# Kernel tuning notes

Measured on AMD Instinct MI355X. Metric: run time of the kernel, lower is better.

The kernel has to match this reference:

```python
import jax, jax.numpy as jnp
import numpy as np

B, DIM, RES, NS, ITERS = 64, 256, 32, 8, 5
NTOK = RES * RES
HID = max(DIM, 128)
EPS = 1e-08
SCALE = DIM ** -0.5


def build_grid(res):
    r = [np.linspace(0.0, 1.0, num=n) for n in (res, res)]
    g = np.stack(np.meshgrid(*r, sparse=False, indexing='ij'), axis=-1)
    g = g.reshape(1, res, res, 2).astype(np.float32)
    return jnp.asarray(np.concatenate([g, 1.0 - g], axis=-1))  # [1,res,res,4]


def ln(x, g, b, eps=1e-5):
    m = x.mean(-1, keepdims=True)
    v = ((x - m) ** 2).mean(-1, keepdims=True)
    return (x - m) / jnp.sqrt(v + eps) * g + b


def ln2(x, g, b, eps=1e-5):  # LayerNorm over last two dims ([ntokens, dim])
    m = x.mean((-2, -1), keepdims=True)
    v = ((x - m) ** 2).mean((-2, -1), keepdims=True)
    return (x - m) / jnp.sqrt(v + eps) * g + b


def lin(x, W, b):
    return x @ W.T + b


def gru_cell(x, h, W_ih, W_hh, b_ih, b_hh):
    gi = x @ W_ih.T + b_ih
    gh = h @ W_hh.T + b_hh
    ir, iz, i_n = jnp.split(gi, 3, axis=-1)
    hr, hz, h_n = jnp.split(gh, 3, axis=-1)
    r = jax.nn.sigmoid(ir + hr)
    z = jax.nn.sigmoid(iz + hz)
    n = jnp.tanh(i_n + r * h_n)
    return (1.0 - z) * n + z * h


def setup_inputs() -> dict:
    key = jax.random.key(0)
    ks = jax.random.split(key, 32)
    p = lambda i, shape, s=0.02: (jax.random.normal(ks[i], shape, dtype=jnp.float32) * s)
    d = {
        'inputs': jax.random.normal(ks[0], (B, DIM, RES, RES), dtype=jnp.float32),
        'init_noise': jax.random.normal(ks[1], (B, NS, DIM), dtype=jnp.float32),
        'W_pos': p(2, (DIM, 4)), 'b_pos': jnp.zeros((DIM,)),
        'g_enc': jnp.ones((NTOK, DIM)), 'b_enc': jnp.zeros((NTOK, DIM)),
        'W_m1': p(3, (DIM, DIM)), 'b_m1': jnp.zeros((DIM,)),
        'W_m2': p(4, (DIM, DIM)), 'b_m2': jnp.zeros((DIM,)),
        'g_in': jnp.ones((DIM,)), 'b_in': jnp.zeros((DIM,)),
        'Wq': p(5, (DIM, DIM)), 'bq': jnp.zeros((DIM,)),
        'Wk': p(6, (DIM, DIM)), 'bk': jnp.zeros((DIM,)),
        'Wv': p(7, (DIM, DIM)), 'bv': jnp.zeros((DIM,)),
        'W_ih': p(8, (3 * DIM, DIM)), 'W_hh': p(9, (3 * DIM, DIM)),
        'b_ih': jnp.zeros((3 * DIM,)), 'b_hh': jnp.zeros((3 * DIM,)),
        'g_s': jnp.ones((DIM,)), 'b_s': jnp.zeros((DIM,)),
        'g_ff': jnp.ones((DIM,)), 'b_ff': jnp.zeros((DIM,)),
        'W_f1': p(10, (HID, DIM)), 'b_f1': jnp.zeros((HID,)),
        'W_f2': p(11, (DIM, HID)), 'b_f2': jnp.zeros((DIM,)),
        'mu': p(12, (1, 1, DIM), 0.1), 'sigma': p(13, (1, 1, DIM), 0.1),
    }
    return d


def _forward(inputs, init_noise, W_pos, b_pos, g_enc, b_enc, W_m1, b_m1, W_m2, b_m2,
             g_in, b_in, Wq, bq, Wk, bk, Wv, bv, W_ih, W_hh, b_ih, b_hh,
             g_s, b_s, g_ff, b_ff, W_f1, b_f1, W_f2, b_f2, mu, sigma):
    grid = build_grid(RES)  # [1,RES,RES,4]
    # encoder transformation (position=True)
    f = jnp.transpose(inputs, (0, 2, 3, 1))               # [B,RES,RES,DIM]
    f = f + lin(grid, W_pos, b_pos)                       # soft position embed
    f = f.reshape(B, NTOK, DIM)
    f = ln2(f, g_enc, b_enc)                              # LayerNorm([ntokens, dim])
    f = jnp.maximum(lin(f, W_m1, b_m1), 0.0)
    f = jnp.maximum(lin(f, W_m2, b_m2), 0.0)
    f = ln(f, g_in, b_in)                                 # norm_input
    k = lin(f, Wk, bk)
    v = lin(f, Wv, bv)

    def step(slots):
        s = ln(slots, g_s, b_s)
        q = lin(s, Wq, bq)
        dots = jnp.einsum('bid,bjd->bij', q, k) * SCALE   # [B,NS,NTOK]
        attn = jax.nn.softmax(dots, axis=1) + EPS         # softmax over slots
        attn = attn / attn.sum(-1, keepdims=True)         # weighted mean
        upd = jnp.einsum('bij,bjd->bid', attn, v)
        ns = gru_cell(upd.reshape(-1, DIM), slots.reshape(-1, DIM),
                      W_ih, W_hh, b_ih, b_hh).reshape(B, NS, DIM)
        h = jnp.maximum(lin(ln(ns, g_ff, b_ff), W_f1, b_f1), 0.0)
        return ns + lin(h, W_f2, b_f2)

    slots = mu + sigma * init_noise
    for _ in range(ITERS):
        slots = step(slots)
    # implicit differentiation: one extra step through detached slots
    slots = step(jax.lax.stop_gradient(slots))
    return slots


def reference(inputs, init_noise, W_pos, b_pos, g_enc, b_enc, W_m1, b_m1, W_m2, b_m2,
              g_in, b_in, Wq, bq, Wk, bk, Wv, bv, W_ih, W_hh, b_ih, b_hh,
              g_s, b_s, g_ff, b_ff, W_f1, b_f1, W_f2, b_f2, mu, sigma):
    return _forward(inputs, init_noise, W_pos, b_pos, g_enc, b_enc, W_m1, b_m1, W_m2, b_m2,
                    g_in, b_in, Wq, bq, Wk, bk, Wv, bv, W_ih, W_hh, b_ih, b_hh,
                    g_s, b_s, g_ff, b_ff, W_f1, b_f1, W_f2, b_f2, mu, sigma)
```

## Files before the change

### kernel.cpp

```cpp
#include <hip/hip_runtime.h>
#include <hip/hip_bf16.h>

#define BB    64
#define DIMN  256
#define NSLOT 8
#define NTOKN 1024
#define NSTEP 6
#define SCALEF 0.0625f

typedef __attribute__((ext_vector_type(8))) short short8;
typedef __attribute__((ext_vector_type(8))) unsigned short ushort8;
typedef __attribute__((ext_vector_type(4))) unsigned short ushort4v;
typedef __attribute__((ext_vector_type(4))) float f32x4;

__device__ __forceinline__ float b2f(unsigned short u) {
  return __uint_as_float((unsigned)u << 16);
}
__device__ __forceinline__ unsigned short f2b(float f) {
  unsigned u = __float_as_uint(f);
  return (unsigned short)((u + 0x7FFFu + ((u >> 16) & 1u)) >> 16);
}

constexpr int kNConv = 31;
constexpr int kConvSizes[kNConv] = {
  131072, 1024, 256, 262144, 262144, 65536, 256, 65536, 256, 256, 256,
  65536, 256, 65536, 256, 65536, 256, 196608, 196608, 768, 768,
  256, 256, 256, 256, 65536, 256, 65536, 256, 256, 256
};
constexpr int kConvTotal = 1513984;

struct PtrPack { const void* p[kNConv]; };

__device__ __forceinline__ float ldin(const void* p, long i, int isbf) {
  if (isbf) return b2f(((const unsigned short*)p)[i]);
  return ((const float*)p)[i];
}

__global__ void detect_dtype(const void* gin, int* flag) {
  unsigned u = *(const unsigned*)gin;
  *flag = (u == 0x3F803F80u) ? 1 : 0;
}

__global__ __launch_bounds__(256) void convert_weights(PtrPack pk, const int* __restrict__ flag,
                                                       float* __restrict__ dst) {
  int idx = blockIdx.x * 256 + threadIdx.x;
  if (idx >= kConvTotal) return;
  int off = idx, a = 0;
  while (a < kNConv - 1 && off >= kConvSizes[a]) { off -= kConvSizes[a]; ++a; }
  dst[idx] = ldin(pk.p[a], off, *flag);
}

constexpr int kWN = 9;
constexpr int kWSize[kWN]  = {65536, 65536, 65536, 65536, 65536, 196608, 196608, 65536, 65536};
constexpr int kWSrc[kWN]   = {656640, 722432, 788736, 854528, 920320, 986112, 1182720, 1381888, 1447680};
constexpr int kWTotal = 851968;

__global__ __launch_bounds__(256) void convert_wbf16(const float* __restrict__ conv,
                                                     unsigned short* __restrict__ wbf) {
  int idx = blockIdx.x * 256 + threadIdx.x;
  if (idx >= kWTotal) return;
  int off = idx, m = 0;
  while (m < kWN - 1 && off >= kWSize[m]) { off -= kWSize[m]; ++m; }
  wbf[idx] = f2b(conv[kWSrc[m] + off]);
}

__global__ __launch_bounds__(256) void posembed_stats(
    const void* __restrict__ in0, const int* __restrict__ flag,
    const float* __restrict__ Wpos, const float* __restrict__ bpos,
    unsigned short* __restrict__ A, float* __restrict__ partials) {
  __shared__ float lds[64 * 65];
  __shared__ float red[8];
  const int tb = blockIdx.x, b = blockIdx.y, tid = threadIdx.x;
  const int t0 = tb * 64;
  const int isbf = *flag;
// ... 62 lines not shown
  int b = threadIdx.x;
  if (b >= BB) return;
  float s = 0.f, q = 0.f;
  for (int i = 0; i < 16; ++i) {
    s += partials[((long)b * 16 + i) * 2];
    q += partials[((long)b * 16 + i) * 2 + 1];
  }
  const float invN = 1.f / (float)(NTOKN * DIMN);
  float m = s * invN;
  float var = q * invN - m * m;
  stats[b * 2] = m;
  stats[b * 2 + 1] = rsqrtf(var + 1e-5f);
}

__global__ __launch_bounds__(256) void ln2_apply(unsigned short* __restrict__ A, const float* __restrict__ stats,
                                                 const float* __restrict__ genc, const float* __restrict__ benc) {
  long i8 = (long)blockIdx.x * 256 + threadIdx.x;
  long i = i8 * 8;
  int b = (int)(i >> 18);
  int td = (int)(i & 262143);
  float m = stats[b * 2], inv = stats[b * 2 + 1];
  ushort8 x = *(const ushort8*)(A + i);
  ushort8 y;
#pragma unroll
  for (int e = 0; e < 8; ++e) {
    float v = (b2f(x[e]) - m) * inv * genc[td + e] + benc[td + e];
    y[e] = f2b(v);
  }
  *(ushort8*)(A + i) = y;
}

__global__ __launch_bounds__(256) void rowln_bf(const unsigned short* __restrict__ X,
                                                const float* __restrict__ g, const float* __restrict__ bb,
                                                unsigned short* __restrict__ Y) {
  const int tid = threadIdx.x, lane = tid & 63;
  const long row = (long)blockIdx.x * 4 + (tid >> 6);
  ushort4v xv = *(const ushort4v*)(X + row * 256 + lane * 4);
  float x0 = b2f(xv[0]), x1 = b2f(xv[1]), x2 = b2f(xv[2]), x3 = b2f(xv[3]);
  float s = x0 + x1 + x2 + x3;
  float q = x0 * x0 + x1 * x1 + x2 * x2 + x3 * x3;
  for (int off = 32; off; off >>= 1) { s += __shfl_xor(s, off); q += __shfl_xor(q, off); }
  float m = s * (1.f / 256.f);
  float inv = rsqrtf(q * (1.f / 256.f) - m * m + 1e-5f);
  float4 gv = *(const float4*)(g + lane * 4);
  float4 bv = *(const float4*)(bb + lane * 4);
  ushort4v y;
  y[0] = f2b((x0 - m) * inv * gv.x + bv.x);
  y[1] = f2b((x1 - m) * inv * gv.y + bv.y);
  y[2] = f2b((x2 - m) * inv * gv.z + bv.z);
  y[3] = f2b((x3 - m) * inv * gv.w + bv.w);
  *(ushort4v*)(Y + row * 256 + lane * 4) = y;
}

template <int ACT, int OUT>
__global__ __launch_bounds__(256) void gemm_tile(
    const unsigned short* __restrict__ X, const unsigned short* __restrict__ W,
    const float* __restrict__ bias, const float* __restrict__ res,
    void* __restrict__ Y, int Nfull) {
  __shared__ unsigned short As[128 * 264];
  __shared__ unsigned short Bs[128 * 264];
  const int tid = threadIdx.x;
  const long m0 = (long)blockIdx.x * 128;
  const int n0 = blockIdx.y * 128;
#pragma unroll
  for (int i = 0; i < 16; ++i) {
    int c = tid + i * 256;
    int row = c >> 5, seg = c & 31;
    *(ushort8*)&As[row * 264 + seg * 8] = *(const ushort8*)(X + (m0 + row) * 256 + seg * 8);
  }
#pragma unroll
  for (int i = 0; i < 16; ++i) {
    int c = tid + i * 256;
    int row = c >> 5, seg = c & 31;
    *(ushort8*)&Bs[row * 264 + seg * 8] = *(const ushort8*)(W + (long)(n0 + row) * 256 + seg * 8);
  }
  __syncthreads();
  const int wave = tid >> 6, lane = tid & 63;
  const int wr = wave >> 1, wc = wave & 1;
  const int lrow = lane & 15, kgrp = lane >> 4;
  f32x4 acc[4][4];
#pragma unroll
  for (int mt = 0; mt < 4; ++mt)
#pragma unroll
    for (int nt = 0; nt < 4; ++nt) acc[mt][nt] = f32x4{0.f, 0.f, 0.f, 0.f};
#pragma unroll
  for (int kc = 0; kc < 8; ++kc) {
    short8 af[4], bf[4];
#pragma unroll
    for (int mt = 0; mt < 4; ++mt)
      af[mt] = *(const short8*)&As[(wr * 64 + mt * 16 + lrow) * 264 + kc * 32 + kgrp * 8];
#pragma unroll
    for (int nt = 0; nt < 4; ++nt)
      bf[nt] = *(const short8*)&Bs[(wc * 64 + nt * 16 + lrow) * 264 + kc * 32 + kgrp * 8];
#pragma unroll
    for (int mt = 0; mt < 4; ++mt)
#pragma unroll
      for (int nt = 0; nt < 4; ++nt)
        acc[mt][nt] = __builtin_amdgcn_mfma_f32_16x16x32_bf16(af[mt], bf[nt], acc[mt][nt], 0, 0, 0);
  }
#pragma unroll
  for (int mt = 0; mt < 4; ++mt)
#pragma unroll
    for (int nt = 0; nt < 4; ++nt) {
      int n = n0 + wc * 64 + nt * 16 + lrow;
      float bn = bias[n];
#pragma unroll
      for (int r = 0; r < 4; ++r) {
        long m = m0 + wr * 64 + mt * 16 + kgrp * 4 + r;
        float v = acc[mt][nt][r] + bn;
        if (ACT) v = fmaxf(v, 0.f);
        if (OUT == 0)      ((unsigned short*)Y)[m * Nfull + n] = f2b(v);
        else if (OUT == 1) ((float*)Y)[m * Nfull + n] = v;
        else               ((float*)Y)[m * Nfull + n] = v + res[m * Nfull + n];
      }
    }
}

__global__ __launch_bounds__(256) void gigh_tile(
    const unsigned short* __restrict__ updb, const unsigned short* __restrict__ sbf,
    const unsigned short* __restrict__ Wih, const unsigned short* __restrict__ Whh,
    const float* __restrict__ bih, const float* __restrict__ bhh,
    float* __restrict__ gib, float* __restrict__ ghb) {
  const unsigned short* X = blockIdx.z ? sbf : updb;
  const unsigned short* W = blockIdx.z ? Whh : Wih;
  const float* bias = blockIdx.z ? bhh : bih;
  float* Y = blockIdx.z ? ghb : gib;
  __shared__ unsigned short As[128 * 264];
  __shared__ unsigned short Bs[128 * 264];
  const int tid = threadIdx.x;
  const long m0 = (long)blockIdx.x * 128;
  const int n0 = blockIdx.y * 128;
#pragma unroll
  for (int i = 0; i < 16; ++i) {
    int c = tid + i * 256;
    int row = c >> 5, seg = c & 31;
    *(ushort8*)&As[row * 264 + seg * 8] = *(const ushort8*)(X + (m0 + row) * 256 + seg * 8);
  }
#pragma unroll
  for (int i = 0; i < 16; ++i) {
    int c = tid + i * 256;
    int row = c >> 5, seg = c & 31;
    *(ushort8*)&Bs[row * 264 + seg * 8] = *(const ushort8*)(W + (long)(n0 + row) * 256 + seg * 8);
  }
  __syncthreads();
  const int wave = tid >> 6, lane = tid & 63;
  const int wr = wave >> 1, wc = wave & 1;
  const int lrow = lane & 15, kgrp = lane >> 4;
  f32x4 acc[4][4];
#pragma unroll
  for (int mt = 0; mt < 4; ++mt)
#pragma unroll
    for (int nt = 0; nt < 4; ++nt) acc[mt][nt] = f32x4{0.f, 0.f, 0.f, 0.f};
#pragma unroll
  for (int kc = 0; kc < 8; ++kc) {
    short8 af[4], bf[4];
#pragma unroll
    for (int mt = 0; mt < 4; ++mt)
      af[mt] = *(const short8*)&As[(wr * 64 + mt * 16 + lrow) * 264 + kc * 32 + kgrp * 8];
#pragma unroll
    for (int nt = 0; nt < 4; ++nt)
      bf[nt] = *(const short8*)&Bs[(wc * 64 + nt * 16 + lrow) * 264 + kc * 32 + kgrp * 8];
#pragma unroll
    for (int mt = 0; mt < 4; ++mt)
#pragma unroll
      for (int nt = 0; nt < 4; ++nt)
        acc[mt][nt] = __builtin_amdgcn_mfma_f32_16x16x32_bf16(af[mt], bf[nt], acc[mt][nt], 0, 0, 0);
  }
#pragma unroll
  for (int mt = 0; mt < 4; ++mt)
#pragma unroll
    for (int nt = 0; nt < 4; ++nt) {
      int n = n0 + wc * 64 + nt * 16 + lrow;
      float bn = bias[n];
#pragma unroll
      for (int r = 0; r < 4; ++r) {
        long m = m0 + wr * 64 + mt * 16 + kgrp * 4 + r;
        Y[m * 768 + n] = acc[mt][nt][r] + bn;
      }
    }
}

__global__ __launch_bounds__(256) void slots_init(const float* __restrict__ noise, const float* __restrict__ mu,
                                                  const float* __restrict__ sigma, float* __restrict__ slots) {
  long i = (long)blockIdx.x * 256 + threadIdx.x;
  int d = (int)(i & 255);
  slots[i] = mu[d] + sigma[d] * noise[i];
}

__global__ __launch_bounds__(256) void lnq_q(
    const float* __restrict__ slots, const float* __restrict__ gs, const float* __restrict__ bs,
    const unsigned short* __restrict__ Wq, const float* __restrict__ bq,
    unsigned short* __restrict__ qb, unsigned short* __restrict__ sbf) {
  __shared__ unsigned short S[16 * 264];
  const int b = blockIdx.x, tid = threadIdx.x;
  const int wave = tid >> 6, lane = tid & 63;
  for (int i = tid; i < 8 * 264; i += 256) S[8 * 264 + i] = 0;
#pragma unroll
  for (int rr = 0; rr < 2; ++rr) {
    int row = wave * 2 + rr;
    float4 xv = *(const float4*)(slots + ((long)b * 8 + row) * 256 + lane * 4);
    float s = xv.x + xv.y + xv.z + xv.w;
    float q = xv.x * xv.x + xv.y * xv.y + xv.z * xv.z + xv.w * xv.w;
    for (int off = 32; off; off >>= 1) { s += __shfl_xor(s, off); q += __shfl_xor(q, off); }
    float m = s * (1.f / 256.f);
    float inv = rsqrtf(q * (1.f / 256.f) - m * m + 1e-5f);
    float4 gv = *(const float4*)(gs + lane * 4);
    float4 bv = *(const float4*)(bs + lane * 4);
    ushort4v y, rb;
    y[0] = f2b((xv.x - m) * inv * gv.x + bv.x);
    y[1] = f2b((xv.y - m) * inv * gv.y + bv.y);
    y[2] = f2b((xv.z - m) * inv * gv.z + bv.z);
    y[3] = f2b((xv.w - m) * inv * gv.w + bv.w);
    rb[0] = f2b(xv.x); rb[1] = f2b(xv.y); rb[2] = f2b(xv.z); rb[3] = f2b(xv.w);
    *(ushort4v*)&S[row * 264 + lane * 4] = y;
    *(ushort4v*)(sbf + ((long)b * 8 + row) * 256 + lane * 4) = rb;
  }
  __syncthreads();
  const int lrow = lane & 15, kgrp = lane >> 4;
  short8 a[8];
#pragma unroll
  for (int kc = 0; kc < 8; ++kc)
    a[kc] = *(const short8*)&S[lrow * 264 + kc * 32 + kgrp * 8];
#pragma unroll
  for (int nt = 0; nt < 4; ++nt) {
    const int n = wave * 64 + nt * 16 + lrow;
    const unsigned short* wp = Wq + (long)n * 256 + kgrp * 8;
    f32x4 acc = {0.f, 0.f, 0.f, 0.f};
#pragma unroll
    for (int kc = 0; kc < 8; ++kc)
      acc = __builtin_amdgcn_mfma_f32_16x16x32_bf16(a[kc], *(const short8*)(wp + kc * 32), acc, 0, 0, 0);
    if (kgrp < 2) {
      float bn = bq[n];
#pragma unroll
      for (int r = 0; r < 4; ++r)
        qb[((long)b * 8 + kgrp * 4 + r) * 256 + n] = f2b(acc[r] + bn);
    }
  }
}

__global__ __launch_bounds__(256) void attn1b(
    const unsigned short* __restrict__ qb, const unsigned short* __restrict__ Kb,
    const unsigned short* __restrict__ Vb,
    float* __restrict__ upd_part, float* __restrict__ asum_part) {
  __shared__ unsigned short Ks[64 * 264];
  __shared__ unsigned short Qs[16 * 264];
  __shared__ float attnS[64 * 8];
  __shared__ float red[4 * 2048];
  const int jt = blockIdx.x, b = blockIdx.y, tid = threadIdx.x;
  const int wave = tid >> 6, lane = tid & 63;
#pragma unroll
  for (int i = 0; i < 8; ++i) {
    int c = tid + i * 256;
    int row = c >> 5, seg = c & 31;
    *(ushort8*)&Ks[row * 264 + seg * 8] =
        *(const ushort8*)(Kb + ((long)(b * NTOKN + jt * 64 + row)) * 256 + seg * 8);
  }
  {
    int row = tid >> 5, seg = tid & 31;
    *(ushort8*)&Qs[row * 264 + seg * 8] = *(const ushort8*)(qb + ((long)(b * 8 + row)) * 256 + seg * 8);
  }
  for (int i = tid; i < 8 * 264; i += 256) Qs[8 * 264 + i] = 0;
  __syncthreads();
  const int lrow = lane & 15, kgrp = lane >> 4;
  f32x4 acc = {0.f, 0.f, 0.f, 0.f};
#pragma unroll
  for (int kc = 0; kc < 8; ++kc) {
    short8 af = *(const short8*)&Ks[(wave * 16 + lrow) * 264 + kc * 32 + kgrp * 8];
    short8 qf = *(const short8*)&Qs[lrow * 264 + kc * 32 + kgrp * 8];
    acc = __builtin_amdgcn_mfma_f32_16x16x32_bf16(af, qf, acc, 0, 0, 0);
  }
  float t0[4], mx[4], e[4], sm[4];
#pragma unroll
  for (int r = 0; r < 4; ++r) { t0[r] = acc[r] * SCALEF; mx[r] = t0[r]; }
#pragma unroll
  for (int msk = 1; msk <= 4; msk <<= 1)
#pragma unroll
    for (int r = 0; r < 4; ++r) mx[r] = fmaxf(mx[r], __shfl_xor(mx[r], msk));
#pragma unroll
  for (int r = 0; r < 4; ++r) { e[r] = expf(t0[r] - mx[r]); sm[r] = e[r]; }
#pragma unroll
  for (int msk = 1; msk <= 4; msk <<= 1)
#pragma unroll
    for (int r = 0; r < 4; ++r) sm[r] += __shfl_xor(sm[r], msk);
  if (lrow < 8) {
#pragma unroll
    for (int r = 0; r < 4; ++r) {
      int jl = wave * 16 + kgrp * 4 + r;
      attnS[jl * 8 + lrow] = e[r] / sm[r] + 1e-8f;
    }
  }
  __syncthreads();
  {
    int s0 = wave * 2;
    float v0 = attnS[lane * 8 + s0], v1 = attnS[lane * 8 + s0 + 1];
    for (int off = 32; off; off >>= 1) { v0 += __shfl_xor(v0, off); v1 += __shfl_xor(v1, off); }
    if (lane == 0) {
      asum_part[((long)(b * 16 + jt)) * 8 + s0] = v0;
      asum_part[((long)(b * 16 + jt)) * 8 + s0 + 1] = v1;
    }
  }
  float au[8][4] = {};
  for (int jl = 0; jl < 16; ++jl) {
    int j = wave * 16 + jl;
    ushort4v v4 = *(const ushort4v*)(Vb + ((long)(b * NTOKN + jt * 64 + j)) * 256 + lane * 4);
    float v0 = b2f(v4[0]), v1 = b2f(v4[1]), v2 = b2f(v4[2]), v3 = b2f(v4[3]);
    float4 a01 = *(const float4*)&attnS[j * 8];
    float4 a23 = *(const float4*)&attnS[j * 8 + 4];
    float aw[8] = {a01.x, a01.y, a01.z, a01.w, a23.x, a23.y, a23.z, a23.w};
#pragma unroll
    for (int s = 0; s < 8; ++s) {
      au[s][0] += aw[s] * v0; au[s][1] += aw[s] * v1;
      au[s][2] += aw[s] * v2; au[s][3] += aw[s] * v3;
    }
  }
#pragma unroll
  for (int s = 0; s < 8; ++s)
    *(float4*)&red[wave * 2048 + s * 256 + lane * 4] = make_float4(au[s][0], au[s][1], au[s][2], au[s][3]);
  __syncthreads();
#pragma unroll
  for (int i = 0; i < 8; ++i) {
    int idx = tid + i * 256;
    float sum = red[idx] + red[2048 + idx] + red[4096 + idx] + red[6144 + idx];
    upd_part[((long)(b * 16 + jt)) * 2048 + idx] = sum;
  }
}

__global__ __launch_bounds__(256) void upd_reduce(
    const float* __restrict__ upd_part, const float* __restrict__ asum_part,
    unsigned short* __restrict__ updb) {
  const int bx = blockIdx.x;
  const int b = bx >> 3, s = bx & 7;
  const int tid = threadIdx.x;
  float as = 0.f;
#pragma unroll
  for (int jt = 0; jt < 16; ++jt) as += asum_part[((long)(b * 16 + jt)) * 8 + s];
  float sum = 0.f;
#pragma unroll
  for (int jt = 0; jt < 16; ++jt)
    sum += upd_part[((long)(b * 16 + jt)) * 2048 + s * 256 + tid];
  updb[((long)b * 8 + s) * 256 + tid] = f2b(sum / as);
}

__global__ __launch_bounds__(256) void gru_ln(const float* __restrict__ gi, const float* __restrict__ gh,
                                              const float* __restrict__ slots,
                                              const float* __restrict__ gff, const float* __restrict__ bff,
                                              float* __restrict__ ns, unsigned short* __restrict__ ffl) {
  const int tid = threadIdx.x, lane = tid & 63;
  const long row = (long)blockIdx.x * 4 + (tid >> 6);
  const int d = lane * 4;
  float4 i1 = *(const float4*)(gi + row * 768 + d);
  float4 i2 = *(const float4*)(gi + row * 768 + 256 + d);
  float4 i3 = *(const float4*)(gi + row * 768 + 512 + d);
  float4 h1 = *(const float4*)(gh + row * 768 + d);
  float4 h2 = *(const float4*)(gh + row * 768 + 256 + d);
  float4 h3 = *(const float4*)(gh + row * 768 + 512 + d);
  float4 sl = *(const float4*)(slots + row * 256 + d);
  float n4[4];
  float r, z, nn;
  r = 1.f / (1.f + expf(-(i1.x + h1.x))); z = 1.f / (1.f + expf(-(i2.x + h2.x)));
  nn = tanhf(i3.x + r * h3.x); n4[0] = (1.f - z) * nn + z * sl.x;
  r = 1.f / (1.f + expf(-(i1.y + h1.y))); z = 1.f / (1.f + expf(-(i2.y + h2.y)));
  nn = tanhf(i3.y + r * h3.y); n4[1] = (1.f - z) * nn + z * sl.y;
  r = 1.f / (1.f + expf(-(i1.z + h1.z))); z = 1.f / (1.f + expf(-(i2.z + h2.z)));
  nn = tanhf(i3.z + r * h3.z); n4[2] = (1.f - z) * nn + z * sl.z;
  r = 1.f / (1.f + expf(-(i1.w + h1.w))); z = 1.f / (1.f + expf(-(i2.w + h2.w)));
  nn = tanhf(i3.w + r * h3.w); n4[3] = (1.f - z) * nn + z * sl.w;
  *(float4*)(ns + row * 256 + d) = make_float4(n4[0], n4[1], n4[2], n4[3]);
  float s = n4[0] + n4[1] + n4[2] + n4[3];
  float q = n4[0] * n4[0] + n4[1] * n4[1] + n4[2] * n4[2] + n4[3] * n4[3];
  for (int off = 32; off; off >>= 1) { s += __shfl_xor(s, off); q += __shfl_xor(q, off); }
  float m = s * (1.f / 256.f);
  float inv = rsqrtf(q * (1.f / 256.f) - m * m + 1e-5f);
  float4 gv = *(const float4*)(gff + d);
  float4 bv = *(const float4*)(bff + d);
  ushort4v y;
  y[0] = f2b((n4[0] - m) * inv * gv.x + bv.x);
  y[1] = f2b((n4[1] - m) * inv * gv.y + bv.y);
  y[2] = f2b((n4[2] - m) * inv * gv.z + bv.z);
  y[3] = f2b((n4[3] - m) * inv * gv.w + bv.w);
  *(ushort4v*)(ffl + row * 256 + d) = y;
}

__global__ __launch_bounds__(256) void write_out(const float* __restrict__ slots, const int* __restrict__ flag,
                                                 void* __restrict__ out) {
  long i = (long)blockIdx.x * 256 + threadIdx.x;
  float v = slots[i];
  if (*flag) ((__hip_bfloat16*)out)[i] = __float2bfloat16(v);
  else ((float*)out)[i] = v;
}

extern "C" void kernel_launch(void* const* d_in, const int* in_sizes, int n_in,
                              void* d_out, int out_size, void* d_ws, size_t ws_size,
                              hipStream_t stream) {
  (void)in_sizes; (void)n_in; (void)out_size; (void)ws_size;
  float* wsf = (float*)d_ws;
  long o = 0;
  float* conv = wsf; o += kConvTotal;
  unsigned short* wbf = (unsigned short*)(wsf + o); o += kWTotal / 2;
  unsigned short* A   = (unsigned short*)(wsf + o); o += (long)BB * NTOKN * DIMN / 2;
  unsigned short* X1  = (unsigned short*)(wsf + o); o += (long)BB * NTOKN * DIMN / 2;
  unsigned short* X2  = (unsigned short*)(wsf + o); o += (long)BB * NTOKN * DIMN / 2;
  unsigned short* Kb  = (unsigned short*)(wsf + o); o += (long)BB * NTOKN * DIMN / 2;
  unsigned short* Vb  = (unsigned short*)(wsf + o); o += (long)BB * NTOKN * DIMN / 2;
  float* slots = wsf + o; o += 131072;
  unsigned short* sbf = (unsigned short*)(wsf + o); o += 65536;
  unsigned short* qb  = (unsigned short*)(wsf + o); o += 65536;
  float* upd_part = wsf + o; o += 2097152;
  float* asum_part = wsf + o; o += 8192;
  unsigned short* updb = (unsigned short*)(wsf + o); o += 65536;
  float* gib   = wsf + o; o += 393216;
  float* ghb   = wsf + o; o += 393216;
  float* nsb   = wsf + o; o += 131072;
  unsigned short* ffl  = (unsigned short*)(wsf + o); o += 65536;
  unsigned short* hbuf = (unsigned short*)(wsf + o); o += 65536;
  float* partials = wsf + o; o += 2048;
  float* stats = wsf + o; o += 128;
  int* flag = (int*)(wsf + o); o += 16;

  long coff[kNConv];
  { long acc = 0; for (int i = 0; i < kNConv; ++i) { coff[i] = acc; acc += kConvSizes[i]; } }
  const float* noise_f = conv + coff[0];
  const float* Wpos = conv + coff[1];
  const float* bpos = conv + coff[2];
  const float* genc = conv + coff[3];
  const float* benc = conv + coff[4];
  const float* bm1  = conv + coff[6];
  const float* bm2  = conv + coff[8];
  const float* gin  = conv + coff[9];
  const float* bin  = conv + coff[10];
  const float* bq   = conv + coff[12];
  const float* bk   = conv + coff[14];
  const float* bv   = conv + coff[16];
  const float* bih  = conv + coff[19];
  const float* bhh  = conv + coff[20];
  const float* gs   = conv + coff[21];
  const float* bs   = conv + coff[22];
  const float* gff  = conv + coff[23];
  const float* bff  = conv + coff[24];
  const float* bf1  = conv + coff[26];
  const float* bf2  = conv + coff[28];
  const float* mu   = conv + coff[29];
  const float* sigma = conv + coff[30];

  const unsigned short* Wm1b = wbf;
  const unsigned short* Wm2b = wbf + 65536;
  const unsigned short* Wqb  = wbf + 131072;
  const unsigned short* Wkb  = wbf + 196608;
  const unsigned short* Wvb  = wbf + 262144;
  const unsigned short* Wihb = wbf + 327680;
  const unsigned short* Whhb = wbf + 524288;
  const unsigned short* Wf1b = wbf + 720896;
  const unsigned short* Wf2b = wbf + 786432;

  detect_dtype<<<1, 1, 0, stream>>>(d_in[10], flag);

  PtrPack pk;
  for (int i = 0; i < kNConv; ++i) pk.p[i] = d_in[i + 1];
  convert_weights<<<(kConvTotal + 255) / 256, 256, 0, stream>>>(pk, flag, conv);
  convert_wbf16<<<(kWTotal + 255) / 256, 256, 0, stream>>>(conv, wbf);

  posembed_stats<<<dim3(16, 64), 256, 0, stream>>>(d_in[0], flag, Wpos, bpos, A, partials);
  stats_reduce<<<1, 64, 0, stream>>>(partials, stats);
  ln2_apply<<<8192, 256, 0, stream>>>(A, stats, genc, benc);
  const int MT = BB * NTOKN / 128;
  gemm_tile<1, 0><<<dim3(MT, 2), 256, 0, stream>>>(A,  Wm1b, bm1, nullptr, X1, 256);
  gemm_tile<1, 0><<<dim3(MT, 2), 256, 0, stream>>>(X1, Wm2b, bm2, nullptr, A,  256);
  rowln_bf<<<BB * NTOKN / 4, 256, 0, stream>>>(A, gin, bin, X2);
  gemm_tile<0, 0><<<dim3(MT, 2), 256, 0, stream>>>(X2, Wkb, bk, nullptr, Kb, 256);
  gemm_tile<0, 0><<<dim3(MT, 2), 256, 0, stream>>>(X2, Wvb, bv, nullptr, Vb, 256);

  slots_init<<<512, 256, 0, stream>>>(noise_f, mu, sigma, slots);

  for (int it = 0; it < NSTEP; ++it) {
    lnq_q<<<64, 256, 0, stream>>>(slots, gs, bs, Wqb, bq, qb, sbf);
    attn1b<<<dim3(16, 64), 256, 0, stream>>>(qb, Kb, Vb, upd_part, asum_part);
    upd_reduce<<<512, 256, 0, stream>>>(upd_part, asum_part, updb);
    gigh_tile<<<dim3(4, 6, 2), 256, 0, stream>>>(updb, sbf, Wihb, Whhb, bih, bhh, gib, ghb);
    gru_ln<<<128, 256, 0, stream>>>(gib, ghb, slots, gff, bff, nsb, ffl);
    gemm_tile<1, 0><<<dim3(4, 2), 256, 0, stream>>>(ffl, Wf1b, bf1, nullptr, hbuf, 256);
    gemm_tile<0, 2><<<dim3(4, 2), 256, 0, stream>>>(hbuf, Wf2b, bf2, nsb, slots, 256);
  }

  write_out<<<512, 256, 0, stream>>>(slots, flag, d_out);
}
```

Baseline: 479.2 us.

## Fuse all slot-attention iterations into one persistent per-batch kernel

Replaces the seven per-iteration launches (q projection, split-token attention, reduction, GRU GEMMs, GRU+LN, two FFN GEMMs) with a single kernel that keeps each batch's slot state in shared memory across all six steps. It also adds a V transpose so the attention-weighted sum runs as an MFMA over tokens. The aim is to remove launch overhead and the global round-trips of intermediates. The cost is that the whole loop runs on only 64 workgroups, so K/V streaming and weight reads lose most of the GPU's parallelism, and the transpose adds an extra pass over V.

Measured after the change: 863.5 us. 1.8x slower.

```diff
diff --git a/kernel.cpp b/kernel.cpp
--- a/kernel.cpp
+++ b/kernel.cpp
@@ -20,6 +20,7 @@
   unsigned u = __float_as_uint(f);
   return (unsigned short)((u + 0x7FFFu + ((u >> 16) & 1u)) >> 16);
 }
+__device__ __forceinline__ float sigm(float x) { return 1.f / (1.f + expf(-x)); }
 
 constexpr int kNConv = 31;
 constexpr int kConvSizes[kNConv] = {
@@ -188,11 +189,10 @@
   *(ushort4v*)(Y + row * 256 + lane * 4) = y;
 }
 
-template <int ACT, int OUT>
+template <int ACT>
 __global__ __launch_bounds__(256) void gemm_tile(
     const unsigned short* __restrict__ X, const unsigned short* __restrict__ W,
-    const float* __restrict__ bias, const float* __restrict__ res,
-    void* __restrict__ Y, int Nfull) {
+    const float* __restrict__ bias, unsigned short* __restrict__ Y) {
   __shared__ unsigned short As[128 * 264];
   __shared__ unsigned short Bs[128 * 264];
   const int tid = threadIdx.x;
@@ -245,284 +245,282 @@
         long m = m0 + wr * 64 + mt * 16 + kgrp * 4 + r;
         float v = acc[mt][nt][r] + bn;
         if (ACT) v = fmaxf(v, 0.f);
-        if (OUT == 0)      ((unsigned short*)Y)[m * Nfull + n] = f2b(v);
-        else if (OUT == 1) ((float*)Y)[m * Nfull + n] = v;
-        else               ((float*)Y)[m * Nfull + n] = v + res[m * Nfull + n];
-      }
-    }
-}
-
-__global__ __launch_bounds__(256) void gigh_tile(
-    const unsigned short* __restrict__ updb, const unsigned short* __restrict__ sbf,
+        Y[m * 256 + n] = f2b(v);
+      }
+    }
+}
+
+__global__ __launch_bounds__(256) void transpose_v(const unsigned short* __restrict__ V,
+                                                   unsigned short* __restrict__ Vt) {
+  __shared__ unsigned short t[64 * 68];
+  const int dt = blockIdx.x, jt = blockIdx.y, b = blockIdx.z, tid = threadIdx.x;
+#pragma unroll
+  for (int i = 0; i < 2; ++i) {
+    int row = (tid >> 3) + i * 32;
+    int c8 = (tid & 7) * 8;
+    ushort8 v = *(const ushort8*)(V + ((long)(b * NTOKN) + jt * 64 + row) * 256 + dt * 64 + c8);
+    ushort4v lo, hi;
+    lo[0] = v[0]; lo[1] = v[1]; lo[2] = v[2]; lo[3] = v[3];
+    hi[0] = v[4]; hi[1] = v[5]; hi[2] = v[6]; hi[3] = v[7];
+    *(ushort4v*)&t[row * 68 + c8] = lo;
+    *(ushort4v*)&t[row * 68 + c8 + 4] = hi;
+  }
+  __syncthreads();
+#pragma unroll
+  for (int i = 0; i < 2; ++i) {
+    int drow = (tid >> 3) + i * 32;
+    int j8 = (tid & 7) * 8;
+    ushort8 y;
+#pragma unroll
+    for (int e = 0; e < 8; ++e) y[e] = t[(j8 + e) * 68 + drow];
+    *(ushort8*)(Vt + ((long)(b * DIMN) + dt * 64 + drow) * NTOKN + jt * 64 + j8) = y;
+  }
+}
+
+__global__ __launch_bounds__(512) void slot_steps(
+    const float* __restrict__ noise, const float* __restrict__ mu, const float* __restrict__ sigma,
+    const float* __restrict__ gs, const float* __restrict__ bs,
+    const unsigned short* __restrict__ Wq, const float* __restrict__ bq,
+    const unsigned short* __restrict__ Kb, const unsigned short* __restrict__ Vt,
     const unsigned short* __restrict__ Wih, const unsigned short* __restrict__ Whh,
     const float* __restrict__ bih, const float* __restrict__ bhh,
-    float* __restrict__ gib, float* __restrict__ ghb) {
-  const unsigned short* X = blockIdx.z ? sbf : updb;
-  const unsigned short* W = blockIdx.z ? Whh : Wih;
-  const float* bias = blockIdx.z ? bhh : bih;
-  float* Y = blockIdx.z ? ghb : gib;
-  __shared__ unsigned short As[128 * 264];
-  __shared__ unsigned short Bs[128 * 264];
-  const int tid = threadIdx.x;
-  const long m0 = (long)blockIdx.x * 128;
-  const int n0 = blockIdx.y * 128;
-#pragma unroll
-  for (int i = 0; i < 16; ++i) {
-    int c = tid + i * 256;
-    int row = c >> 5, seg = c & 31;
-    *(ushort8*)&As[row * 264 + seg * 8] = *(const ushort8*)(X + (m0 + row) * 256 + seg * 8);
-  }
-#pragma unroll
-  for (int i = 0; i < 16; ++i) {
-    int c = tid + i * 256;
-    int row = c >> 5, seg = c & 31;
-    *(ushort8*)&Bs[row * 264 + seg * 8] = *(const ushort8*)(W + (long)(n0 + row) * 256 + seg * 8);
-  }
-  __syncthreads();
-  const int wave = tid >> 6, lane = tid & 63;
-  const int wr = wave >> 1, wc = wave & 1;
-  const int lrow = lane & 15, kgrp = lane >> 4;
-  f32x4 acc[4][4];
-#pragma unroll
-  for (int mt = 0; mt < 4; ++mt)
-#pragma unroll
-    for (int nt = 0; nt < 4; ++nt) acc[mt][nt] = f32x4{0.f, 0.f, 0.f, 0.f};
-#pragma unroll
-  for (int kc = 0; kc < 8; ++kc) {
-    short8 af[4], bf[4];
-#pragma unroll
-    for (int mt = 0; mt < 4; ++mt)
-      af[mt] = *(const short8*)&As[(wr * 64 + mt * 16 + lrow) * 264 + kc * 32 + kgrp * 8];
-#pragma unroll
-    for (int nt = 0; nt < 4; ++nt)
-      bf[nt] = *(const short8*)&Bs[(wc * 64 + nt * 16 + lrow) * 264 + kc * 32 + kgrp * 8];
-#pragma unroll
-    for (int mt = 0; mt < 4; ++mt)
-#pragma unroll
-      for (int nt = 0; nt < 4; ++nt)
-        acc[mt][nt] = __builtin_amdgcn_mfma_f32_16x16x32_bf16(af[mt], bf[nt], acc[mt][nt], 0, 0, 0);
-  }
-#pragma unroll
-  for (int mt = 0; mt < 4; ++mt)
-#pragma unroll
-    for (int nt = 0; nt < 4; ++nt) {
-      int n = n0 + wc * 64 + nt * 16 + lrow;
-      float bn = bias[n];
-#pragma unroll
-      for (int r = 0; r < 4; ++r) {
-        long m = m0 + wr * 64 + mt * 16 + kgrp * 4 + r;
-        Y[m * 768 + n] = acc[mt][nt][r] + bn;
-      }
-    }
-}
-
-__global__ __launch_bounds__(256) void slots_init(const float* __restrict__ noise, const float* __restrict__ mu,
-                                                  const float* __restrict__ sigma, float* __restrict__ slots) {
-  long i = (long)blockIdx.x * 256 + threadIdx.x;
-  int d = (int)(i & 255);
-  slots[i] = mu[d] + sigma[d] * noise[i];
-}
-
-__global__ __launch_bounds__(256) void lnq_q(
-    const float* __restrict__ slots, const float* __restrict__ gs, const float* __restrict__ bs,
-    const unsigned short* __restrict__ Wq, const float* __restrict__ bq,
-    unsigned short* __restrict__ qb, unsigned short* __restrict__ sbf) {
-  __shared__ unsigned short S[16 * 264];
+    const float* __restrict__ gff, const float* __restrict__ bff,
+    const unsigned short* __restrict__ Wf1, const float* __restrict__ bf1,
+    const unsigned short* __restrict__ Wf2, const float* __restrict__ bf2,
+    const int* __restrict__ flag, void* __restrict__ out) {
+  __shared__ float state[8][264];
+  __shared__ float nsS[8][264];
+  __shared__ unsigned short slnQ[16 * 264];
+  __shared__ unsigned short qQ[16 * 264];
+  __shared__ unsigned short sbfQ[16 * 264];
+  __shared__ unsigned short updQ[16 * 264];
+  __shared__ unsigned short fflQ[16 * 264];
+  __shared__ unsigned short hQ[16 * 264];
+  __shared__ unsigned short attnT[16 * 1032];
+  __shared__ float red[64];
   const int b = blockIdx.x, tid = threadIdx.x;
   const int wave = tid >> 6, lane = tid & 63;
-  for (int i = tid; i < 8 * 264; i += 256) S[8 * 264 + i] = 0;
-#pragma unroll
-  for (int rr = 0; rr < 2; ++rr) {
-    int row = wave * 2 + rr;
-    float4 xv = *(const float4*)(slots + ((long)b * 8 + row) * 256 + lane * 4);
-    float s = xv.x + xv.y + xv.z + xv.w;
-    float q = xv.x * xv.x + xv.y * xv.y + xv.z * xv.z + xv.w * xv.w;
-    for (int off = 32; off; off >>= 1) { s += __shfl_xor(s, off); q += __shfl_xor(q, off); }
-    float m = s * (1.f / 256.f);
-    float inv = rsqrtf(q * (1.f / 256.f) - m * m + 1e-5f);
-    float4 gv = *(const float4*)(gs + lane * 4);
-    float4 bv = *(const float4*)(bs + lane * 4);
-    ushort4v y, rb;
-    y[0] = f2b((xv.x - m) * inv * gv.x + bv.x);
-    y[1] = f2b((xv.y - m) * inv * gv.y + bv.y);
-    y[2] = f2b((xv.z - m) * inv * gv.z + bv.z);
-    y[3] = f2b((xv.w - m) * inv * gv.w + bv.w);
-    rb[0] = f2b(xv.x); rb[1] = f2b(xv.y); rb[2] = f2b(xv.z); rb[3] = f2b(xv.w);
-    *(ushort4v*)&S[row * 264 + lane * 4] = y;
-    *(ushort4v*)(sbf + ((long)b * 8 + row) * 256 + lane * 4) = rb;
+  const int lrow = lane & 15, kgrp = lane >> 4;
+  for (int i = tid; i < 8 * 264; i += 512) {
+    slnQ[8 * 264 + i] = 0; qQ[8 * 264 + i] = 0; sbfQ[8 * 264 + i] = 0;
+    updQ[8 * 264 + i] = 0; fflQ[8 * 264 + i] = 0; hQ[8 * 264 + i] = 0;
+  }
+  for (int i = tid; i < 16 * 1032; i += 512) attnT[i] = 0;
+  {
+    int idx = tid * 4;
+    int row = idx >> 8, d = idx & 255;
+    float4 nv = *(const float4*)(noise + (long)b * 2048 + idx);
+    float4 mv = *(const float4*)(mu + d);
+    float4 sv = *(const float4*)(sigma + d);
+    state[row][d + 0] = mv.x + sv.x * nv.x;
+    state[row][d + 1] = mv.y + sv.y * nv.y;
+    state[row][d + 2] = mv.z + sv.z * nv.z;
+    state[row][d + 3] = mv.w + sv.w * nv.w;
   }
   __syncthreads();
-  const int lrow = lane & 15, kgrp = lane >> 4;
-  short8 a[8];
-#pragma unroll
-  for (int kc = 0; kc < 8; ++kc)
-    a[kc] = *(const short8*)&S[lrow * 264 + kc * 32 + kgrp * 8];
-#pragma unroll
-  for (int nt = 0; nt < 4; ++nt) {
-    const int n = wave * 64 + nt * 16 + lrow;
-    const unsigned short* wp = Wq + (long)n * 256 + kgrp * 8;
-    f32x4 acc = {0.f, 0.f, 0.f, 0.f};
-#pragma unroll
-    for (int kc = 0; kc < 8; ++kc)
-      acc = __builtin_amdgcn_mfma_f32_16x16x32_bf16(a[kc], *(const short8*)(wp + kc * 32), acc, 0, 0, 0);
-    if (kgrp < 2) {
-      float bn = bq[n];
-#pragma unroll
-      for (int r = 0; r < 4; ++r)
-        qb[((long)b * 8 + kgrp * 4 + r) * 256 + n] = f2b(acc[r] + bn);
-    }
-  }
-}
-
-__global__ __launch_bounds__(256) void attn1b(
-    const unsigned short* __restrict__ qb, const unsigned short* __restrict__ Kb,
-    const unsigned short* __restrict__ Vb,
-    float* __restrict__ upd_part, float* __restrict__ asum_part) {
-  __shared__ unsigned short Ks[64 * 264];
-  __shared__ unsigned short Qs[16 * 264];
-  __shared__ float attnS[64 * 8];
-  __shared__ float red[4 * 2048];
-  const int jt = blockIdx.x, b = blockIdx.y, tid = threadIdx.x;
-  const int wave = tid >> 6, lane = tid & 63;
-#pragma unroll
-  for (int i = 0; i < 8; ++i) {
-    int c = tid + i * 256;
-    int row = c >> 5, seg = c & 31;
-    *(ushort8*)&Ks[row * 264 + seg * 8] =
-        *(const ushort8*)(Kb + ((long)(b * NTOKN + jt * 64 + row)) * 256 + seg * 8);
+
+  for (int it = 0; it < NSTEP; ++it) {
+    {
+      int row = wave;
+      float4 xv = *(float4*)&state[row][lane * 4];
+      float s = xv.x + xv.y + xv.z + xv.w;
+      float q = xv.x * xv.x + xv.y * xv.y + xv.z * xv.z + xv.w * xv.w;
+      for (int off = 32; off; off >>= 1) { s += __shfl_xor(s, off); q += __shfl_xor(q, off); }
+      float m = s * (1.f / 256.f);
+      float inv = rsqrtf(q * (1.f / 256.f) - m * m + 1e-5f);
+      float4 gv = *(const float4*)(gs + lane * 4);
+      float4 bv = *(const float4*)(bs + lane * 4);
+      ushort4v y, rb;
+      y[0] = f2b((xv.x - m) * inv * gv.x + bv.x);
+      y[1] = f2b((xv.y - m) * inv * gv.y + bv.y);
+      y[2] = f2b((xv.z - m) * inv * gv.z + bv.z);
+      y[3] = f2b((xv.w - m) * inv * gv.w + bv.w);
+      rb[0] = f2b(xv.x); rb[1] = f2b(xv.y); rb[2] = f2b(xv.z); rb[3] = f2b(xv.w);
+      *(ushort4v*)&slnQ[row * 264 + lane * 4] = y;
+      *(ushort4v*)&sbfQ[row * 264 + lane * 4] = rb;
+    }
+    __syncthreads();
+#pragma unroll
+    for (int nt2 = 0; nt2 < 2; ++nt2) {
+      int n = wave * 32 + nt2 * 16 + lrow;
+      f32x4 acc = {0.f, 0.f, 0.f, 0.f};
+#pragma unroll
+      for (int kc = 0; kc < 8; ++kc) {
+        short8 af = *(const short8*)&slnQ[lrow * 264 + kgrp * 8 + kc * 32];
+        short8 wf = *(const short8*)(Wq + (long)n * 256 + kgrp * 8 + kc * 32);
+        acc = __builtin_amdgcn_mfma_f32_16x16x32_bf16(af, wf, acc, 0, 0, 0);
+      }
+      if (kgrp < 2) {
+        float bn = bq[n];
+#pragma unroll
+        for (int r = 0; r < 4; ++r)
+          qQ[(kgrp * 4 + r) * 264 + n] = f2b(acc[r] + bn);
+      }
+    }
+    __syncthreads();
+    {
+      float asum_r = 0.f;
+#pragma unroll
+      for (int jj = 0; jj < 2; ++jj) {
+        int jt = wave + jj * 8;
+#pragma unroll
+        for (int tt = 0; tt < 4; ++tt) {
+          int jbase = jt * 64 + tt * 16;
+          f32x4 acc = {0.f, 0.f, 0.f, 0.f};
+#pragma unroll
+          for (int kc = 0; kc < 8; ++kc) {
+            short8 kf = *(const short8*)(Kb + ((long)(b * NTOKN) + jbase + lrow) * 256 + kgrp * 8 + kc * 32);
+            short8 qf = *(const short8*)&qQ[lrow * 264 + kgrp * 8 + kc * 32];
+            acc = __builtin_amdgcn_mfma_f32_16x16x32_bf16(kf, qf, acc, 0, 0, 0);
+          }
+          float t0[4], mx[4], e[4], sm[4];
+#pragma unroll
+          for (int r = 0; r < 4; ++r) { t0[r] = acc[r] * SCALEF; mx[r] = t0[r]; }
+#pragma unroll
+          for (int msk = 1; msk <= 4; msk <<= 1)
+#pragma unroll
+            for (int r = 0; r < 4; ++r) mx[r] = fmaxf(mx[r], __shfl_xor(mx[r], msk));
+#pragma unroll
+          for (int r = 0; r < 4; ++r) { e[r] = expf(t0[r] - mx[r]); sm[r] = e[r]; }
+#pragma unroll
+          for (int msk = 1; msk <= 4; msk <<= 1)
+#pragma unroll
+            for (int r = 0; r < 4; ++r) sm[r] += __shfl_xor(sm[r], msk);
+          if (lrow < 8) {
+#pragma unroll
+            for (int r = 0; r < 4; ++r) {
+              unsigned short ab = f2b(e[r] / sm[r] + 1e-8f);
+              attnT[lrow * 1032 + jbase + kgrp * 4 + r] = ab;
+              asum_r += b2f(ab);
+            }
+          }
+        }
+      }
+      asum_r += __shfl_xor(asum_r, 16);
+      asum_r += __shfl_xor(asum_r, 32);
+      if (kgrp == 0 && lrow < 8) red[wave * 8 + lrow] = asum_r;
+    }
+    __syncthreads();
+#pragma unroll
+    for (int nt2 = 0; nt2 < 2; ++nt2) {
+      int d = (wave * 2 + nt2) * 16 + lrow;
+      f32x4 acc = {0.f, 0.f, 0.f, 0.f};
+#pragma unroll
+      for (int kc = 0; kc < 32; ++kc) {
+        short8 af = *(const short8*)&attnT[lrow * 1032 + kgrp * 8 + kc * 32];
+        short8 vf = *(const short8*)(Vt + ((long)(b * DIMN) + d) * NTOKN + kgrp * 8 + kc * 32);
+        acc = __builtin_amdgcn_mfma_f32_16x16x32_bf16(af, vf, acc, 0, 0, 0);
+      }
+      if (kgrp < 2) {
+#pragma unroll
+        for (int r = 0; r < 4; ++r) {
+          int s = kgrp * 4 + r;
+          float as = red[s] + red[8 + s] + red[16 + s] + red[24 + s]
+                   + red[32 + s] + red[40 + s] + red[48 + s] + red[56 + s];
+          updQ[s * 264 + d] = f2b(acc[r] / as);
+        }
+      }
+    }
+    __syncthreads();
+#pragma unroll
+    for (int nt2 = 0; nt2 < 2; ++nt2) {
+      int n = wave * 32 + nt2 * 16 + lrow;
+      f32x4 gir = {0.f,0.f,0.f,0.f}, giz = {0.f,0.f,0.f,0.f}, gin_ = {0.f,0.f,0.f,0.f};
+      f32x4 ghr = {0.f,0.f,0.f,0.f}, ghz = {0.f,0.f,0.f,0.f}, ghn = {0.f,0.f,0.f,0.f};
+#pragma unroll
+      for (int kc = 0; kc < 8; ++kc) {
+        short8 uf = *(const short8*)&updQ[lrow * 264 + kgrp * 8 + kc * 32];
+        short8 sf = *(const short8*)&sbfQ[lrow * 264 + kgrp * 8 + kc * 32];
+        int ko = kgrp * 8 + kc * 32;
+        gir = __builtin_amdgcn_mfma_f32_16x16x32_bf16(uf, *(const short8*)(Wih + (long)n * 256 + ko), gir, 0, 0, 0);
+        giz = __builtin_amdgcn_mfma_f32_16x16x32_bf16(uf, *(const short8*)(Wih + (long)(n + 256) * 256 + ko), giz, 0, 0, 0);
+        gin_ = __builtin_amdgcn_mfma_f32_16x16x32_bf16(uf, *(const short8*)(Wih + (long)(n + 512) * 256 + ko), gin_, 0, 0, 0);
+        ghr = __builtin_amdgcn_mfma_f32_16x16x32_bf16(sf, *(const short8*)(Whh + (long)n * 256 + ko), ghr, 0, 0, 0);
+        ghz = __builtin_amdgcn_mfma_f32_16x16x32_bf16(sf, *(const short8*)(Whh + (long)(n + 256) * 256 + ko), ghz, 0, 0, 0);
+        ghn = __builtin_amdgcn_mfma_f32_16x16x32_bf16(sf, *(const short8*)(Whh + (long)(n + 512) * 256 + ko), ghn, 0, 0, 0);
+      }
+      if (kgrp < 2) {
+        float br = bih[n], bz = bih[n + 256], bnn = bih[n + 512];
+        float hr = bhh[n], hz = bhh[n + 256], hnn = bhh[n + 512];
+#pragma unroll
+        for (int r = 0; r < 4; ++r) {
+          int row = kgrp * 4 + r;
+          float rr = sigm((gir[r] + br) + (ghr[r] + hr));
+          float zz = sigm((giz[r] + bz) + (ghz[r] + hz));
+          float nn = tanhf((gin_[r] + bnn) + rr * (ghn[r] + hnn));
+          nsS[row][n] = (1.f - zz) * nn + zz * state[row][n];
+        }
+      }
+    }
+    __syncthreads();
+    {
+      int row = wave;
+      float4 xv = *(float4*)&nsS[row][lane * 4];
+      float s = xv.x + xv.y + xv.z + xv.w;
+      float q = xv.x * xv.x + xv.y * xv.y + xv.z * xv.z + xv.w * xv.w;
+      for (int off = 32; off; off >>= 1) { s += __shfl_xor(s, off); q += __shfl_xor(q, off); }
+      float m = s * (1.f / 256.f);
+      float inv = rsqrtf(q * (1.f / 256.f) - m * m + 1e-5f);
+      float4 gv = *(const float4*)(gff + lane * 4);
+      float4 bv = *(const float4*)(bff + lane * 4);
+      ushort4v y;
+      y[0] = f2b((xv.x - m) * inv * gv.x + bv.x);
+      y[1] = f2b((xv.y - m) * inv * gv.y + bv.y);
+      y[2] = f2b((xv.z - m) * inv * gv.z + bv.z);
+      y[3] = f2b((xv.w - m) * inv * gv.w + bv.w);
+      *(ushort4v*)&fflQ[row * 264 + lane * 4] = y;
+    }
+    __syncthreads();
+#pragma unroll
+    for (int nt2 = 0; nt2 < 2; ++nt2) {
+      int n = wave * 32 + nt2 * 16 + lrow;
+      f32x4 acc = {0.f, 0.f, 0.f, 0.f};
+#pragma unroll
+      for (int kc = 0; kc < 8; ++kc) {
+        short8 af = *(const short8*)&fflQ[lrow * 264 + kgrp * 8 + kc * 32];
+        short8 wf = *(const short8*)(Wf1 + (long)n * 256 + kgrp * 8 + kc * 32);
+        acc = __builtin_amdgcn_mfma_f32_16x16x32_bf16(af, wf, acc, 0, 0, 0);
+      }
+      if (kgrp < 2) {
+        float bn = bf1[n];
+#pragma unroll
+        for (int r = 0; r < 4; ++r)
+          hQ[(kgrp * 4 + r) * 264 + n] = f2b(fmaxf(acc[r] + bn, 0.f));
+      }
+    }
+    __syncthreads();
+#pragma unroll
+    for (int nt2 = 0; nt2 < 2; ++nt2) {
+      int n = wave * 32 + nt2 * 16 + lrow;
+      f32x4 acc = {0.f, 0.f, 0.f, 0.f};
+#pragma unroll
+      for (int kc = 0; kc < 8; ++kc) {
+        short8 af = *(const short8*)&hQ[lrow * 264 + kgrp * 8 + kc * 32];
+        short8 wf = *(const short8*)(Wf2 + (long)n * 256 + kgrp * 8 + kc * 32);
+        acc = __builtin_amdgcn_mfma_f32_16x16x32_bf16(af, wf, acc, 0, 0, 0);
+      }
+      if (kgrp < 2) {
+        float bn = bf2[n];
+#pragma unroll
+        for (int r = 0; r < 4; ++r) {
+          int row = kgrp * 4 + r;
+          state[row][n] = acc[r] + bn + nsS[row][n];
+        }
+      }
+    }
+    __syncthreads();
   }
   {
-    int row = tid >> 5, seg = tid & 31;
-    *(ushort8*)&Qs[row * 264 + seg * 8] = *(const ushort8*)(qb + ((long)(b * 8 + row)) * 256 + seg * 8);
-  }
-  for (int i = tid; i < 8 * 264; i += 256) Qs[8 * 264 + i] = 0;
-  __syncthreads();
-  const int lrow = lane & 15, kgrp = lane >> 4;
-  f32x4 acc = {0.f, 0.f, 0.f, 0.f};
-#pragma unroll
-  for (int kc = 0; kc < 8; ++kc) {
-    short8 af = *(const short8*)&Ks[(wave * 16 + lrow) * 264 + kc * 32 + kgrp * 8];
-    short8 qf = *(const short8*)&Qs[lrow * 264 + kc * 32 + kgrp * 8];
-    acc = __builtin_amdgcn_mfma_f32_16x16x32_bf16(af, qf, acc, 0, 0, 0);
-  }
-  float t0[4], mx[4], e[4], sm[4];
-#pragma unroll
-  for (int r = 0; r < 4; ++r) { t0[r] = acc[r] * SCALEF; mx[r] = t0[r]; }
-#pragma unroll
-  for (int msk = 1; msk <= 4; msk <<= 1)
-#pragma unroll
-    for (int r = 0; r < 4; ++r) mx[r] = fmaxf(mx[r], __shfl_xor(mx[r], msk));
-#pragma unroll
-  for (int r = 0; r < 4; ++r) { e[r] = expf(t0[r] - mx[r]); sm[r] = e[r]; }
-#pragma unroll
-  for (int msk = 1; msk <= 4; msk <<= 1)
-#pragma unroll
-    for (int r = 0; r < 4; ++r) sm[r] += __shfl_xor(sm[r], msk);
-  if (lrow < 8) {
-#pragma unroll
-    for (int r = 0; r < 4; ++r) {
-      int jl = wave * 16 + kgrp * 4 + r;
-      attnS[jl * 8 + lrow] = e[r] / sm[r] + 1e-8f;
-    }
-  }
-  __syncthreads();
-  {
-    int s0 = wave * 2;
-    float v0 = attnS[lane * 8 + s0], v1 = attnS[lane * 8 + s0 + 1];
-    for (int off = 32; off; off >>= 1) { v0 += __shfl_xor(v0, off); v1 += __shfl_xor(v1, off); }
-    if (lane == 0) {
-      asum_part[((long)(b * 16 + jt)) * 8 + s0] = v0;
-      asum_part[((long)(b * 16 + jt)) * 8 + s0 + 1] = v1;
-    }
-  }
-  float au[8][4] = {};
-  for (int jl = 0; jl < 16; ++jl) {
-    int j = wave * 16 + jl;
-    ushort4v v4 = *(const ushort4v*)(Vb + ((long)(b * NTOKN + jt * 64 + j)) * 256 + lane * 4);
-    float v0 = b2f(v4[0]), v1 = b2f(v4[1]), v2 = b2f(v4[2]), v3 = b2f(v4[3]);
-    float4 a01 = *(const float4*)&attnS[j * 8];
-    float4 a23 = *(const float4*)&attnS[j * 8 + 4];
-    float aw[8] = {a01.x, a01.y, a01.z, a01.w, a23.x, a23.y, a23.z, a23.w};
-#pragma unroll
-    for (int s = 0; s < 8; ++s) {
-      au[s][0] += aw[s] * v0; au[s][1] += aw[s] * v1;
-      au[s][2] += aw[s] * v2; au[s][3] += aw[s] * v3;
-    }
-  }
-#pragma unroll
-  for (int s = 0; s < 8; ++s)
-    *(float4*)&red[wave * 2048 + s * 256 + lane * 4] = make_float4(au[s][0], au[s][1], au[s][2], au[s][3]);
-  __syncthreads();
-#pragma unroll
-  for (int i = 0; i < 8; ++i) {
-    int idx = tid + i * 256;
-    float sum = red[idx] + red[2048 + idx] + red[4096 + idx] + red[6144 + idx];
-    upd_part[((long)(b * 16 + jt)) * 2048 + idx] = sum;
-  }
-}
-
-__global__ __launch_bounds__(256) void upd_reduce(
-    const float* __restrict__ upd_part, const float* __restrict__ asum_part,
-    unsigned short* __restrict__ updb) {
-  const int bx = blockIdx.x;
-  const int b = bx >> 3, s = bx & 7;
-  const int tid = threadIdx.x;
-  float as = 0.f;
-#pragma unroll
-  for (int jt = 0; jt < 16; ++jt) as += asum_part[((long)(b * 16 + jt)) * 8 + s];
-  float sum = 0.f;
-#pragma unroll
-  for (int jt = 0; jt < 16; ++jt)
-    sum += upd_part[((long)(b * 16 + jt)) * 2048 + s * 256 + tid];
-  updb[((long)b * 8 + s) * 256 + tid] = f2b(sum / as);
-}
-
-__global__ __launch_bounds__(256) void gru_ln(const float* __restrict__ gi, const float* __restrict__ gh,
-                                              const float* __restrict__ slots,
-                                              const float* __restrict__ gff, const float* __restrict__ bff,
-                                              float* __restrict__ ns, unsigned short* __restrict__ ffl) {
-  const int tid = threadIdx.x, lane = tid & 63;
-  const long row = (long)blockIdx.x * 4 + (tid >> 6);
-  const int d = lane * 4;
-  float4 i1 = *(const float4*)(gi + row * 768 + d);
-  float4 i2 = *(const float4*)(gi + row * 768 + 256 + d);
-  float4 i3 = *(const float4*)(gi + row * 768 + 512 + d);
-  float4 h1 = *(const float4*)(gh + row * 768 + d);
-  float4 h2 = *(const float4*)(gh + row * 768 + 256 + d);
-  float4 h3 = *(const float4*)(gh + row * 768 + 512 + d);
-  float4 sl = *(const float4*)(slots + row * 256 + d);
-  float n4[4];
-  float r, z, nn;
-  r = 1.f / (1.f + expf(-(i1.x + h1.x))); z = 1.f / (1.f + expf(-(i2.x + h2.x)));
-  nn = tanhf(i3.x + r * h3.x); n4[0] = (1.f - z) * nn + z * sl.x;
-  r = 1.f / (1.f + expf(-(i1.y + h1.y))); z = 1.f / (1.f + expf(-(i2.y + h2.y)));
-  nn = tanhf(i3.y + r * h3.y); n4[1] = (1.f - z) * nn + z * sl.y;
-  r = 1.f / (1.f + expf(-(i1.z + h1.z))); z = 1.f / (1.f + expf(-(i2.z + h2.z)));
-  nn = tanhf(i3.z + r * h3.z); n4[2] = (1.f - z) * nn + z * sl.z;
-  r = 1.f / (1.f + expf(-(i1.w + h1.w))); z = 1.f / (1.f + expf(-(i2.w + h2.w)));
-  nn = tanhf(i3.w + r * h3.w); n4[3] = (1.f - z) * nn + z * sl.w;
-  *(float4*)(ns + row * 256 + d) = make_float4(n4[0], n4[1], n4[2], n4[3]);
-  float s = n4[0] + n4[1] + n4[2] + n4[3];
-  float q = n4[0] * n4[0] + n4[1] * n4[1] + n4[2] * n4[2] + n4[3] * n4[3];
-  for (int off = 32; off; off >>= 1) { s += __shfl_xor(s, off); q += __shfl_xor(q, off); }
-  float m = s * (1.f / 256.f);
-  float inv = rsqrtf(q * (1.f / 256.f) - m * m + 1e-5f);
-  float4 gv = *(const float4*)(gff + d);
-  float4 bv = *(const float4*)(bff + d);
-  ushort4v y;
-  y[0] = f2b((n4[0] - m) * inv * gv.x + bv.x);
-  y[1] = f2b((n4[1] - m) * inv * gv.y + bv.y);
-  y[2] = f2b((n4[2] - m) * inv * gv.z + bv.z);
-  y[3] = f2b((n4[3] - m) * inv * gv.w + bv.w);
-  *(ushort4v*)(ffl + row * 256 + d) = y;
-}
-
-__global__ __launch_bounds__(256) void write_out(const float* __restrict__ slots, const int* __restrict__ flag,
-                                                 void* __restrict__ out) {
-  long i = (long)blockIdx.x * 256 + threadIdx.x;
-  float v = slots[i];
-  if (*flag) ((__hip_bfloat16*)out)[i] = __float2bfloat16(v);
-  else ((float*)out)[i] = v;
+    int idx = tid * 4;
+    int row = idx >> 8, d = idx & 255;
+    int isbf = *flag;
+#pragma unroll
+    for (int e = 0; e < 4; ++e) {
+      float v = state[row][d + e];
+      if (isbf) ((__hip_bfloat16*)out)[(long)b * 2048 + idx + e] = __float2bfloat16(v);
+      else ((float*)out)[(long)b * 2048 + idx + e] = v;
+    }
+  }
 }
 
 extern "C" void kernel_launch(void* const* d_in, const int* in_sizes, int n_in,
@@ -538,17 +536,7 @@
   unsigned short* X2  = (unsigned short*)(wsf + o); o += (long)BB * NTOKN * DIMN / 2;
   unsigned short* Kb  = (unsigned short*)(wsf + o); o += (long)BB * NTOKN * DIMN / 2;
   unsigned short* Vb  = (unsigned short*)(wsf + o); o += (long)BB * NTOKN * DIMN / 2;
-  float* slots = wsf + o; o += 131072;
-  unsigned short* sbf = (unsigned short*)(wsf + o); o += 65536;
-  unsigned short* qb  = (unsigned short*)(wsf + o); o += 65536;
-  float* upd_part = wsf + o; o += 2097152;
-  float* asum_part = wsf + o; o += 8192;
-  unsigned short* updb = (unsigned short*)(wsf + o); o += 65536;
-  float* gib   = wsf + o; o += 393216;
-  float* ghb   = wsf + o; o += 393216;
-  float* nsb   = wsf + o; o += 131072;
-  unsigned short* ffl  = (unsigned short*)(wsf + o); o += 65536;
-  unsigned short* hbuf = (unsigned short*)(wsf + o); o += 65536;
+  unsigned short* Vt  = (unsigned short*)(wsf + o); o += (long)BB * NTOKN * DIMN / 2;
   float* partials = wsf + o; o += 2048;
   float* stats = wsf + o; o += 128;
   int* flag = (int*)(wsf + o); o += 16;
@@ -599,23 +587,14 @@
   stats_reduce<<<1, 64, 0, stream>>>(partials, stats);
   ln2_apply<<<8192, 256, 0, stream>>>(A, stats, genc, benc);
   const int MT = BB * NTOKN / 128;
-  gemm_tile<1, 0><<<dim3(MT, 2), 256, 0, stream>>>(A,  Wm1b, bm1, nullptr, X1, 256);
-  gemm_tile<1, 0><<<dim3(MT, 2), 256, 0, stream>>>(X1, Wm2b, bm2, nullptr, A,  256);
+  gemm_tile<1><<<dim3(MT, 2), 256, 0, stream>>>(A,  Wm1b, bm1, X1);
+  gemm_tile<1><<<dim3(MT, 2), 256, 0, stream>>>(X1, Wm2b, bm2, A);
   rowln_bf<<<BB * NTOKN / 4, 256, 0, stream>>>(A, gin, bin, X2);
-  gemm_tile<0, 0><<<dim3(MT, 2), 256, 0, stream>>>(X2, Wkb, bk, nullptr, Kb, 256);
-  gemm_tile<0, 0><<<dim3(MT, 2), 256, 0, stream>>>(X2, Wvb, bv, nullptr, Vb, 256);
-
-  slots_init<<<512, 256, 0, stream>>>(noise_f, mu, sigma, slots);
-
-  for (int it = 0; it < NSTEP; ++it) {
-    lnq_q<<<64, 256, 0, stream>>>(slots, gs, bs, Wqb, bq, qb, sbf);
-    attn1b<<<dim3(16, 64), 256, 0, stream>>>(qb, Kb, Vb, upd_part, asum_part);
-    upd_reduce<<<512, 256, 0, stream>>>(upd_part, asum_part, updb);
-    gigh_tile<<<dim3(4, 6, 2), 256, 0, stream>>>(updb, sbf, Wihb, Whhb, bih, bhh, gib, ghb);
-    gru_ln<<<128, 256, 0, stream>>>(gib, ghb, slots, gff, bff, nsb, ffl);
-    gemm_tile<1, 0><<<dim3(4, 2), 256, 0, stream>>>(ffl, Wf1b, bf1, nullptr, hbuf, 256);
-    gemm_tile<0, 2><<<dim3(4, 2), 256, 0, stream>>>(hbuf, Wf2b, bf2, nsb, slots, 256);
-  }
-
-  write_out<<<512, 256, 0, stream>>>(slots, flag, d_out);
-}
+  gemm_tile<0><<<dim3(MT, 2), 256, 0, stream>>>(X2, Wkb, bk, Kb);
+  gemm_tile<0><<<dim3(MT, 2), 256, 0, stream>>>(X2, Wvb, bv, Vb);
+  transpose_v<<<dim3(4, 16, 64), 256, 0, stream>>>(Vb, Vt);
+
+  slot_steps<<<64, 512, 0, stream>>>(
+      noise_f, mu, sigma, gs, bs, Wqb, bq, Kb, Vt,
+      Wihb, Whhb, bih, bhh, gff, bff, Wf1b, bf1, Wf2b, bf2, flag, d_out);
+}
```
